# Optimization experiments

Measured on AMD Instinct MI355X. Metric: run time of the kernel, lower is better.

The kernel has to match this reference:

```python
import jax, jax.numpy as jnp
import numpy as np

N_E, E_DIM, N = 1024, 128, 262144


def setup_inputs() -> dict:
    key = jax.random.key(0)
    kx, kw = jax.random.split(key)
    x = jax.random.normal(kx, (N, E_DIM), dtype=jnp.float32)
    # nn.Embedding weight initialized uniform(-1/n_e, 1/n_e)
    W = jax.random.uniform(kw, (N_E, E_DIM), dtype=jnp.float32,
                           minval=-1.0 / N_E, maxval=1.0 / N_E)
    return {"x": x, "W": W}


def reference(x, W):
    # d[n, k] = ||x_n||^2 + ||W_k||^2 - 2 x_n . W_k   -> shape [N, n_e]
    d = (jnp.sum(x * x, axis=1, keepdims=True)
         + jnp.sum(W * W, axis=1)
         - 2.0 * jnp.matmul(x, W.T))
    min_indices = jnp.argmin(d, axis=1)          # [N] int
    z_q = jnp.take(W, min_indices, axis=0)       # [N, e_dim] gather
    return (z_q, min_indices)
```

## Files before the change

kernel.cpp:

```cpp
#include <hip/hip_runtime.h>

#define EDIM 128
#define NE   1024
#define TAU  5e-5f
#define CAPP 65536

typedef short v8s __attribute__((ext_vector_type(8)));
typedef float v4f __attribute__((ext_vector_type(4)));
typedef __attribute__((address_space(3))) void       lds_t;
typedef const __attribute__((address_space(1))) void gm_t;

__device__ inline unsigned bf16_rne(float f) {
    unsigned u = __float_as_uint(f);
    return (u + 0x7fffu + ((u >> 16) & 1u)) >> 16;
}
__device__ inline float bf16_tof(unsigned h) { return __uint_as_float(h << 16); }

__global__ void vq_prep(const float* __restrict__ W,
                        unsigned short* __restrict__ whiF,
                        unsigned short* __restrict__ wloF,
                        float* __restrict__ Wt,
                        float* __restrict__ swsq_ws)
{
#pragma clang fp contract(off)
    const int t = blockIdx.x * 256 + threadIdx.x;
    #pragma unroll
    for (int rep = 0; rep < 2; ++rep) {
        int i = t + rep * 65536;
        float v = W[i];
        int code = i >> 7, k = i & 127;
        int sub = code >> 4, m = code & 15;
        int ks = k >> 5, g = (k >> 3) & 3, e = k & 7;
        int o = sub * 2048 + ks * 512 + (g * 16 + m) * 8 + e;
        unsigned h = bf16_rne(v);
        whiF[o] = (unsigned short)h;
        wloF[o] = (unsigned short)bf16_rne(v - bf16_tof(h));
        int o2 = t + rep * 65536;
        Wt[o2] = W[(o2 & 1023) * EDIM + (o2 >> 10)];
    }
    if (t < NE) {
        const float4* wr = reinterpret_cast<const float4*>(W) + (size_t)t * 32;
        float4 A = wr[0], B = wr[1];
        float r0 = A.x*A.x, r1 = A.y*A.y, r2 = A.z*A.z, r3 = A.w*A.w;
        float r4 = B.x*B.x, r5 = B.y*B.y, r6 = B.z*B.z, r7 = B.w*B.w;
        #pragma unroll
        for (int i = 2; i < 32; i += 2) {
            float4 C = wr[i], D = wr[i + 1];
            r0 += C.x*C.x; r1 += C.y*C.y; r2 += C.z*C.z; r3 += C.w*C.w;
            r4 += D.x*D.x; r5 += D.y*D.y; r6 += D.z*D.z; r7 += D.w*D.w;
        }
        swsq_ws[t] = ((r0 + r1) + (r2 + r3)) + ((r4 + r5) + (r6 + r7));
    }
}

union SMem {
    struct { unsigned short ring[3][2][4096]; float snwk2h[NE]; } p1;
    struct { float4 scan[2048]; int sbest[128]; } p2;
};

__global__ __launch_bounds__(256, 3) void vq_mfma9(
    const float* __restrict__ x,
    const unsigned short* __restrict__ whiF, const unsigned short* __restrict__ wloF,
    const float* __restrict__ W, const float* __restrict__ swsq_ws,
    float* __restrict__ zq, float* __restrict__ idxout,
    int* __restrict__ cnt_pair, int* __restrict__ cnt_full,
    int* __restrict__ plist, int* __restrict__ flist)
{
    __shared__ SMem sm;

    const int tid = threadIdx.x;
    const int wid = tid >> 6;
    const int l   = tid & 63;
    const int m   = l & 15;
    const int g   = l >> 4;

    const long long row0 = (long long)blockIdx.x * 128;
    const float4* x4 = reinterpret_cast<const float4*>(x);
    const float4* W4 = reinterpret_cast<const float4*>(W);

#define STAGE_TILE(T, B) do {                                                          \
    __builtin_amdgcn_global_load_lds((gm_t*)(whiF + (size_t)(T) * 4096 + tid * 8),     \
        (lds_t*)&sm.p1.ring[B][0][tid * 8], 16, 0, 0);                                 \
    __builtin_amdgcn_global_load_lds((gm_t*)(whiF + (size_t)(T) * 4096 + 2048 + tid * 8), \
        (lds_t*)&sm.p1.ring[B][0][2048 + tid * 8], 16, 0, 0);                          \
    __builtin_amdgcn_global_load_lds((gm_t*)(wloF + (size_t)(T) * 4096 + tid * 8),     \
        (lds_t*)&sm.p1.ring[B][1][tid * 8], 16, 0, 0);                                 \
    __builtin_amdgcn_global_load_lds((gm_t*)(wloF + (size_t)(T) * 4096 + 2048 + tid * 8), \
        (lds_t*)&sm.p1.ring[B][1][2048 + tid * 8], 16, 0, 0);                          \
} while (0)

    STAGE_TILE(0, 0);
    STAGE_TILE(1, 1);

    {
        float4 v = reinterpret_cast<const float4*>(swsq_ws)[tid];
        v.x *= -0.5f; v.y *= -0.5f; v.z *= -0.5f; v.w *= -0.5f;
        reinterpret_cast<float4*>(sm.p1.snwk2h)[tid] = v;
    }

    const long long rA0 = row0 + wid * 32 + m;
    const long long rA1 = rA0 + 16;
    v8s a0h[4], a0l[4], a1h[4], a1l[4];
    #pragma unroll
    for (int ks = 0; ks < 4; ++ks) {
        float4 p0 = x4[rA0 * 32 + ks * 8 + g * 2];
        float4 p1 = x4[rA0 * 32 + ks * 8 + g * 2 + 1];
        float4 q0 = x4[rA1 * 32 + ks * 8 + g * 2];
        float4 q1 = x4[rA1 * 32 + ks * 8 + g * 2 + 1];
        float vp[8] = {p0.x,p0.y,p0.z,p0.w,p1.x,p1.y,p1.z,p1.w};
        float vq[8] = {q0.x,q0.y,q0.z,q0.w,q1.x,q1.y,q1.z,q1.w};
        #pragma unroll
        for (int e = 0; e < 8; ++e) {
            unsigned h0 = bf16_rne(vp[e]);
            a0h[ks][e] = (short)h0;
            a0l[ks][e] = (short)bf16_rne(vp[e] - bf16_tof(h0));
            unsigned h1 = bf16_rne(vq[e]);
            a1h[ks][e] = (short)h1;
            a1l[ks][e] = (short)bf16_rne(vq[e] - bf16_tof(h1));
        }
    }
    __syncthreads();

    float best[8], sec[8]; int bk[8];
    #pragma unroll
    for (int r = 0; r < 8; ++r) { best[r] = -3.4e38f; sec[r] = -3.4e38f; bk[r] = 0; }

    int bcur = 0;
    #pragma unroll 1
    for (int t = 0; t < 32; ++t) {
        if (t + 1 < 32) asm volatile("s_waitcnt vmcnt(4)" ::: "memory");
        else            asm volatile("s_waitcnt vmcnt(0)" ::: "memory");
        __builtin_amdgcn_s_barrier();

        if (t + 2 < 32) {
            int bnext = bcur + 2; if (bnext >= 3) bnext -= 3;
            STAGE_TILE(t + 2, bnext);
        }

        const unsigned short* bh_base = &sm.p1.ring[bcur][0][l * 8];
        const unsigned short* bl_base = &sm.p1.ring[bcur][1][l * 8];

        #pragma unroll
        for (int half = 0; half < 2; ++half) {
            const int k = t * 32 + half * 16 + m;
            const int hb = half * 2048;
            v8s bh0 = *(const v8s*)(bh_base + hb);
            v8s bh1 = *(const v8s*)(bh_base + hb + 512);
            v8s bh2 = *(const v8s*)(bh_base + hb + 1024);
            v8s bh3 = *(const v8s*)(bh_base + hb + 1536);
            v8s bl0 = *(const v8s*)(bl_base + hb);
            v8s bl1 = *(const v8s*)(bl_base + hb + 512);
            v8s bl2 = *(const v8s*)(bl_base + hb + 1024);
            v8s bl3 = *(const v8s*)(bl_base + hb + 1536);

            const float h = sm.p1.snwk2h[k];
            v4f acc0 = {h, h, h, h};
            v4f acc1 = {h, h, h, h};
            __builtin_amdgcn_s_setprio(1);
            acc0 = __builtin_amdgcn_mfma_f32_16x16x32_bf16(a0h[0], bh0, acc0, 0, 0, 0);
            acc0 = __builtin_amdgcn_mfma_f32_16x16x32_bf16(a0l[0], bh0, acc0, 0, 0, 0);
            acc0 = __builtin_amdgcn_mfma_f32_16x16x32_bf16(a0h[0], bl0, acc0, 0, 0, 0);
            acc1 = __builtin_amdgcn_mfma_f32_16x16x32_bf16(a1h[0], bh0, acc1, 0, 0, 0);
            acc1 = __builtin_amdgcn_mfma_f32_16x16x32_bf16(a1l[0], bh0, acc1, 0, 0, 0);
            acc1 = __builtin_amdgcn_mfma_f32_16x16x32_bf16(a1h[0], bl0, acc1, 0, 0, 0);
            acc0 = __builtin_amdgcn_mfma_f32_16x16x32_bf16(a0h[1], bh1, acc0, 0, 0, 0);
            acc0 = __builtin_amdgcn_mfma_f32_16x16x32_bf16(a0l[1], bh1, acc0, 0, 0, 0);
            acc0 = __builtin_amdgcn_mfma_f32_16x16x32_bf16(a0h[1], bl1, acc0, 0, 0, 0);
            acc1 = __builtin_amdgcn_mfma_f32_16x16x32_bf16(a1h[1], bh1, acc1, 0, 0, 0);
            acc1 = __builtin_amdgcn_mfma_f32_16x16x32_bf16(a1l[1], bh1, acc1, 0, 0, 0);
            acc1 = __builtin_amdgcn_mfma_f32_16x16x32_bf16(a1h[1], bl1, acc1, 0, 0, 0);
            acc0 = __builtin_amdgcn_mfma_f32_16x16x32_bf16(a0h[2], bh2, acc0, 0, 0, 0);
            acc0 = __builtin_amdgcn_mfma_f32_16x16x32_bf16(a0l[2], bh2, acc0, 0, 0, 0);
            acc0 = __builtin_amdgcn_mfma_f32_16x16x32_bf16(a0h[2], bl2, acc0, 0, 0, 0);
            acc1 = __builtin_amdgcn_mfma_f32_16x16x32_bf16(a1h[2], bh2, acc1, 0, 0, 0);
            acc1 = __builtin_amdgcn_mfma_f32_16x16x32_bf16(a1l[2], bh2, acc1, 0, 0, 0);
            acc1 = __builtin_amdgcn_mfma_f32_16x16x32_bf16(a1h[2], bl2, acc1, 0, 0, 0);
            acc0 = __builtin_amdgcn_mfma_f32_16x16x32_bf16(a0h[3], bh3, acc0, 0, 0, 0);
            acc0 = __builtin_amdgcn_mfma_f32_16x16x32_bf16(a0l[3], bh3, acc0, 0, 0, 0);
            acc0 = __builtin_amdgcn_mfma_f32_16x16x32_bf16(a0h[3], bl3, acc0, 0, 0, 0);
            acc1 = __builtin_amdgcn_mfma_f32_16x16x32_bf16(a1h[3], bh3, acc1, 0, 0, 0);
            acc1 = __builtin_amdgcn_mfma_f32_16x16x32_bf16(a1l[3], bh3, acc1, 0, 0, 0);
            acc1 = __builtin_amdgcn_mfma_f32_16x16x32_bf16(a1h[3], bl3, acc1, 0, 0, 0);
            __builtin_amdgcn_s_setprio(0);

            #pragma unroll
            for (int r = 0; r < 4; ++r) {
                float b0 = best[r];
                float a0r = acc0[r];
                sec[r]  = __builtin_amdgcn_fmed3f(a0r, b0, sec[r]);
                bk[r]   = (a0r > b0) ? k : bk[r];
                best[r] = fmaxf(b0, a0r);
                float b1 = best[4 + r];
                float a1r = acc1[r];
                sec[4+r]  = __builtin_amdgcn_fmed3f(a1r, b1, sec[4+r]);
                bk[4+r]   = (a1r > b1) ? k : bk[4+r];
                best[4+r] = fmaxf(b1, a1r);
            }
        }

        bcur = (bcur == 2) ? 0 : bcur + 1;
    }
    __syncthreads();

    #pragma unroll
    for (int r = 0; r < 8; ++r) {
        int rowL = wid * 32 + ((r >> 2) << 4) + (g << 2) + (r & 3);
        float4 e;
        e.x = -2.f * best[r]; e.y = -2.f * sec[r];
        e.z = __int_as_float(bk[r]); e.w = 0.f;
        sm.p2.scan[rowL * 16 + m] = e;
    }
    __syncthreads();

    if (tid < 128) {
        const int stag = tid & 7;
        float b1 = 3.4e38f; int k1 = 0x7fffffff;
        #pragma unroll 1
        for (int mm = 0; mm < 16; ++mm) {
            float4 e = sm.p2.scan[tid * 16 + (mm ^ stag)];
            int kk = __float_as_int(e.z);
            if (e.x < b1 || (e.x == b1 && kk < k1)) { b1 = e.x; k1 = kk; }
        }
        const float th = b1 + TAU;
        int nb = 0; bool asec = false;
        float b2 = 3.4e38f; int k2 = 0x7fffffff;
        #pragma unroll 1
        for (int mm = 0; mm < 16; ++mm) {
            float4 e = sm.p2.scan[tid * 16 + (mm ^ stag)];
            int kk = __float_as_int(e.z);
            nb  += (e.x <= th) ? 1 : 0;
            asec = asec || (e.y <= th);
            if (kk != k1 && (e.x < b2 || (e.x == b2 && kk < k2))) { b2 = e.x; k2 = kk; }
        }
        sm.p2.sbest[tid] = k1;
        idxout[row0 + tid] = (float)k1;
        const int row = (int)(row0 + tid);
        if (asec || nb > 2) {
            int s2 = atomicAdd(cnt_full, 1);
            flist[s2] = row;
        } else if (nb == 2) {
            int slot = atomicAdd(cnt_pair, 1);
            if (slot < CAPP) { plist[2 * slot] = row; plist[2 * slot + 1] = k2; }
            else { int s2 = atomicAdd(cnt_full, 1); flist[s2] = row; }
        }
    }
    __syncthreads();

    float4* zq4 = reinterpret_cast<float4*>(zq);
    for (int i = tid; i < 128 * 32; i += 256) {
        int r = i >> 5, c4 = i & 31;
        zq4[row0 * 32 + i] = W4[(size_t)sm.p2.sbest[r] * 32 + c4];
    }
#undef STAGE_TILE
}

__global__ __launch_bounds__(256, 4) void vq_fix(
    const float* __restrict__ x, const float* __restrict__ W,
    const float* __restrict__ Wt, const float* __restrict__ swsq_ws,
    float* __restrict__ zq, float* __restrict__ idxout,
    const int* __restrict__ cnt_pair, const int* __restrict__ plist,
    const int* __restrict__ cnt_full, const int* __restrict__ flist)
{
#pragma clang fp contract(off)
    const float4* W4 = reinterpret_cast<const float4*>(W);
    float4* zq4 = reinterpret_cast<float4*>(zq);

    {
        int n = *cnt_pair; if (n > CAPP) n = CAPP;
        const int gsz = gridDim.x * 256;
        for (int i = blockIdx.x * 256 + threadIdx.x; i < n; i += gsz) {
            const int row = plist[2 * i];
            const int k2  = plist[2 * i + 1];
            const int k1  = (int)idxout[row];
            const float4* xr4 = reinterpret_cast<const float4*>(x + (size_t)row * EDIM);
            float4 A = xr4[0], B = xr4[1];
            float r0 = A.x*A.x, r1 = A.y*A.y, r2 = A.z*A.z, r3 = A.w*A.w;
            float r4 = B.x*B.x, r5 = B.y*B.y, r6 = B.z*B.z, r7 = B.w*B.w;
            #pragma unroll
            for (int q = 2; q < 32; q += 2) {
                float4 C = xr4[q], D = xr4[q + 1];
                r0 += C.x*C.x; r1 += C.y*C.y; r2 += C.z*C.z; r3 += C.w*C.w;
                r4 += D.x*D.x; r5 += D.y*D.y; r6 += D.z*D.z; r7 += D.w*D.w;
            }
            float xxv = ((r0 + r1) + (r2 + r3)) + ((r4 + r5) + (r6 + r7));
            const float* xr = x + (size_t)row * EDIM;
            const float* w1 = W + (size_t)k1 * EDIM;
            const float* w2 = W + (size_t)k2 * EDIM;
            float dot1 = 0.f, dot2 = 0.f;
            #pragma unroll 4
            for (int j = 0; j < EDIM; ++j) {
                float a = xr[j];
                dot1 = fmaf(a, w1[j], dot1);
                dot2 = fmaf(a, w2[j], dot2);
            }
            float d1 = (xxv + swsq_ws[k1]) - (dot1 + dot1);
            float d2 = (xxv + swsq_ws[k2]) - (dot2 + dot2);
            int kw = (d2 < d1 || (d2 == d1 && k2 < k1)) ? k2 : k1;
            if (kw != k1) {
                idxout[row] = (float)kw;
                const float4* wr = W4 + (size_t)kw * 32;
                float4* zr = zq4 + (size_t)row * 32;
                #pragma unroll
                for (int q = 0; q < 32; ++q) zr[q] = wr[q];
            }
        }
    }

    {
        const int nf = *cnt_full;
        const int lane = threadIdx.x & 63;
        const int nw = gridDim.x * 4;
        const float4* Wt4 = reinterpret_cast<const float4*>(Wt);
        for (int i = blockIdx.x * 4 + (threadIdx.x >> 6); i < nf; i += nw) {
            const long long row = flist[i];
            const float4* xr4 = reinterpret_cast<const float4*>(x + row * EDIM);
            float xxv;
            {
                float4 A = xr4[0], B = xr4[1];
                float r0 = A.x*A.x, r1 = A.y*A.y, r2 = A.z*A.z, r3 = A.w*A.w;
                float r4 = B.x*B.x, r5 = B.y*B.y, r6 = B.z*B.z, r7 = B.w*B.w;
                #pragma unroll
                for (int q = 2; q < 32; q += 2) {
                    float4 C = xr4[q], D = xr4[q + 1];
                    r0 += C.x*C.x; r1 += C.y*C.y; r2 += C.z*C.z; r3 += C.w*C.w;
                    r4 += D.x*D.x; r5 += D.y*D.y; r6 += D.z*D.z; r7 += D.w*D.w;
                }
                xxv = ((r0 + r1) + (r2 + r3)) + ((r4 + r5) + (r6 + r7));
            }
            float acc[4][4];
            #pragma unroll
            for (int c = 0; c < 4; ++c)
                #pragma unroll
                for (int e = 0; e < 4; ++e) acc[c][e] = 0.f;
            const float* xr = x + row * EDIM;
            #pragma unroll 4
            for (int j = 0; j < EDIM; ++j) {
                float a = xr[j];
                #pragma unroll
                for (int c = 0; c < 4; ++c) {
                    float4 w = Wt4[(size_t)j * 256 + c * 64 + lane];
                    acc[c][0] = fmaf(a, w.x, acc[c][0]);
                    acc[c][1] = fmaf(a, w.y, acc[c][1]);
                    acc[c][2] = fmaf(a, w.z, acc[c][2]);
                    acc[c][3] = fmaf(a, w.w, acc[c][3]);
                }
            }
            float dbest = 3.4e38f; int bkk = 0;
            #pragma unroll
            for (int c = 0; c < 4; ++c)
                #pragma unroll
                for (int e = 0; e < 4; ++e) {
                    int k = c * 256 + lane * 4 + e;
                    float t1 = xxv + swsq_ws[k];
                    float d  = t1 - (acc[c][e] + acc[c][e]);
                    if (d < dbest) { dbest = d; bkk = k; }
                }
            #pragma unroll
            for (int mk = 1; mk < 64; mk <<= 1) {
                float od = __shfl_xor(dbest, mk);
                int   ok = __shfl_xor(bkk, mk);
                if (od < dbest || (od == dbest && ok < bkk)) { dbest = od; bkk = ok; }
            }
            if (lane == 0) idxout[row] = (float)bkk;
            if (lane < 32) zq4[row * 32 + lane] = W4[(size_t)bkk * 32 + lane];
        }
    }
}

__global__ __launch_bounds__(64, 2) void vq_v4(
    const float* __restrict__ x, const float* __restrict__ W,
    float* __restrict__ zq, float* __restrict__ idxout)
{
#pragma clang fp contract(off)
    __shared__ float swsq[NE];
    __shared__ int   sbest[64];
    const int tid = threadIdx.x;
    const long long row0 = (long long)blockIdx.x * 64;
    const long long row  = row0 + tid;
    const float4* x4 = reinterpret_cast<const float4*>(x);
    const float4* W4 = reinterpret_cast<const float4*>(W);
    float4 xr[32];
    #pragma unroll
    for (int i = 0; i < 32; ++i) xr[i] = x4[row * 32 + i];
    #pragma unroll
    for (int i = 0; i < 32; ++i)
        asm volatile("" : "+v"(xr[i].x), "+v"(xr[i].y), "+v"(xr[i].z), "+v"(xr[i].w));
    for (int k = tid; k < NE; k += 64) {
        const float4* wr = W4 + (size_t)k * 32;
        float4 A = wr[0], B = wr[1];
        float r0 = A.x*A.x, r1 = A.y*A.y, r2 = A.z*A.z, r3 = A.w*A.w;
        float r4 = B.x*B.x, r5 = B.y*B.y, r6 = B.z*B.z, r7 = B.w*B.w;
        #pragma unroll
        for (int i = 2; i < 32; i += 2) {
            float4 C = wr[i], D = wr[i + 1];
            r0 += C.x*C.x; r1 += C.y*C.y; r2 += C.z*C.z; r3 += C.w*C.w;
            r4 += D.x*D.x; r5 += D.y*D.y; r6 += D.z*D.z; r7 += D.w*D.w;
        }
        swsq[k] = ((r0 + r1) + (r2 + r3)) + ((r4 + r5) + (r6 + r7));
    }
    float xxv;
    {
        float r0 = xr[0].x*xr[0].x, r1 = xr[0].y*xr[0].y;
        float r2 = xr[0].z*xr[0].z, r3 = xr[0].w*xr[0].w;
        float r4 = xr[1].x*xr[1].x, r5 = xr[1].y*xr[1].y;
        float r6 = xr[1].z*xr[1].z, r7 = xr[1].w*xr[1].w;
        #pragma unroll
        for (int i = 2; i < 32; i += 2) {
            r0 += xr[i].x*xr[i].x;     r1 += xr[i].y*xr[i].y;
            r2 += xr[i].z*xr[i].z;     r3 += xr[i].w*xr[i].w;
            r4 += xr[i+1].x*xr[i+1].x; r5 += xr[i+1].y*xr[i+1].y;
            r6 += xr[i+1].z*xr[i+1].z; r7 += xr[i+1].w*xr[i+1].w;
        }
        xxv = ((r0 + r1) + (r2 + r3)) + ((r4 + r5) + (r6 + r7));
    }
    __syncthreads();
    float dbest = 3.4e38f; int bestk = 0;
    #pragma unroll 1
    for (int k0 = 0; k0 < NE; k0 += 8) {
        float acc[8];
        #pragma unroll
        for (int c = 0; c < 8; ++c) acc[c] = 0.f;
        #pragma unroll
        for (int j4 = 0; j4 < 32; ++j4) {
            const float4 a = xr[j4];
            #pragma unroll
            for (int c = 0; c < 8; ++c) {
                float4 w = W4[(size_t)(k0 + c) * 32 + j4];
                acc[c] = fmaf(a.x, w.x, acc[c]); acc[c] = fmaf(a.y, w.y, acc[c]);
                acc[c] = fmaf(a.z, w.z, acc[c]); acc[c] = fmaf(a.w, w.w, acc[c]);
            }
        }
        #pragma unroll
        for (int c = 0; c < 8; ++c) {
            float t1 = xxv + swsq[k0 + c];
            float d  = t1 - (acc[c] + acc[c]);
            if (d < dbest) { dbest = d; bestk = k0 + c; }
        }
    }
    sbest[tid] = bestk;
    idxout[row] = (float)bestk;
    __syncthreads();
    float4* zq4 = reinterpret_cast<float4*>(zq);
    for (int i = tid; i < 64 * 32; i += 64) {
        int r = i >> 5, c4 = i & 31;
        zq4[row0 * 32 + i] = W4[(size_t)sbest[r] * 32 + c4];
    }
}

extern "C" void kernel_launch(void* const* d_in, const int* in_sizes, int n_in,
                              void* d_out, int out_size, void* d_ws, size_t ws_size,
                              hipStream_t stream) {
    (void)n_in; (void)out_size;
    const float* x = (const float*)d_in[0];
    const float* W = (const float*)d_in[1];
    const int Nrows = in_sizes[0] / EDIM;

    float* zqp    = (float*)d_out;
    float* idxout = zqp + (size_t)Nrows * EDIM;

    const size_t need = 16 + 2 * (size_t)NE * EDIM * 2 + NE * 4
                      + (size_t)NE * EDIM * 4 + (size_t)CAPP * 2 * 4
                      + (size_t)Nrows * 4;
    if (ws_size < need) {
        vq_v4<<<dim3(Nrows / 64), dim3(64), 0, stream>>>(x, W, zqp, idxout);
        return;
    }

    char* p = (char*)d_ws;
    int*            cnt_pair = (int*)p;
    int*            cnt_full = (int*)(p + 4);
    unsigned short* whiF  = (unsigned short*)(p + 16);
    unsigned short* wloF  = whiF + NE * EDIM;
    float*          swsqw = (float*)(wloF + NE * EDIM);
    float*          Wt    = swsqw + NE;
    int*            plist = (int*)(Wt + NE * EDIM);
    int*            flist = plist + CAPP * 2;

    hipMemsetAsync(d_ws, 0, 16, stream);
    vq_prep<<<dim3(256), dim3(256), 0, stream>>>(W, whiF, wloF, Wt, swsqw);
    vq_mfma9<<<dim3(Nrows / 128), dim3(256), 0, stream>>>(x, whiF, wloF, W, swsqw,
                                                          zqp, idxout,
                                                          cnt_pair, cnt_full,
                                                          plist, flist);
    vq_fix<<<dim3(1024), dim3(256), 0, stream>>>(x, W, Wt, swsqw, zqp, idxout,
                                                 cnt_pair, plist, cnt_full, flist);
}
```

Baseline: 330.9 us.

## Halve codebook tile size to raise occupancy and coalesce prep layout writes

The main kernel now stages 16 codes per pipeline step instead of 32, halving the LDS ring and shrinking the argmin scratch (float4 to float2 plus a separate int array), so launch bounds can request 4 blocks per CU instead of 3. The loop runs 64 iterations with one MFMA group each, which doubles the barrier and wait overhead per code. Separately, the prep kernel builds the bf16 hi/lo swizzled layout through shared memory with vector stores instead of scattered 2-byte global writes. Fewer registers may be available per thread under the higher occupancy target.

```diff
diff --git a/kernel.cpp b/kernel.cpp
--- a/kernel.cpp
+++ b/kernel.cpp
@@ -23,21 +23,38 @@
                         float* __restrict__ swsq_ws)
 {
 #pragma clang fp contract(off)
-    const int t = blockIdx.x * 256 + threadIdx.x;
+    __shared__ unsigned short lh[2048], ll[2048];
+    const int tid = threadIdx.x;
+    const int t = blockIdx.x * 256 + tid;
+
+    if (blockIdx.x < 64) {
+        const int sub = blockIdx.x;
+        const int dst = ((tid & 15) >> 2) * 512 + (tid & 3) * 128 + (tid >> 4) * 8;
+        float4 p0 = reinterpret_cast<const float4*>(W)[sub * 512 + tid * 2];
+        float4 p1 = reinterpret_cast<const float4*>(W)[sub * 512 + tid * 2 + 1];
+        float v[8] = {p0.x,p0.y,p0.z,p0.w,p1.x,p1.y,p1.z,p1.w};
+        v8s hh, llw;
+        #pragma unroll
+        for (int j = 0; j < 8; ++j) {
+            unsigned h = bf16_rne(v[j]);
+            hh[j]  = (short)h;
+            llw[j] = (short)bf16_rne(v[j] - bf16_tof(h));
+        }
+        *reinterpret_cast<v8s*>(&lh[dst]) = hh;
+        *reinterpret_cast<v8s*>(&ll[dst]) = llw;
+        __syncthreads();
+        *reinterpret_cast<v8s*>(&whiF[sub * 2048 + tid * 8]) =
+            *reinterpret_cast<const v8s*>(&lh[tid * 8]);
+        *reinterpret_cast<v8s*>(&wloF[sub * 2048 + tid * 8]) =
+            *reinterpret_cast<const v8s*>(&ll[tid * 8]);
+    }
+
     #pragma unroll
     for (int rep = 0; rep < 2; ++rep) {
-        int i = t + rep * 65536;
-        float v = W[i];
-        int code = i >> 7, k = i & 127;
-        int sub = code >> 4, m = code & 15;
-        int ks = k >> 5, g = (k >> 3) & 3, e = k & 7;
-        int o = sub * 2048 + ks * 512 + (g * 16 + m) * 8 + e;
-        unsigned h = bf16_rne(v);
-        whiF[o] = (unsigned short)h;
-        wloF[o] = (unsigned short)bf16_rne(v - bf16_tof(h));
         int o2 = t + rep * 65536;
         Wt[o2] = W[(o2 & 1023) * EDIM + (o2 >> 10)];
     }
+
     if (t < NE) {
         const float4* wr = reinterpret_cast<const float4*>(W) + (size_t)t * 32;
         float4 A = wr[0], B = wr[1];
@@ -54,11 +71,11 @@
 }
 
 union SMem {
-    struct { unsigned short ring[3][2][4096]; float snwk2h[NE]; } p1;
-    struct { float4 scan[2048]; int sbest[128]; } p2;
+    struct { unsigned short ring[3][2][2048]; float snwk2h[NE]; } p1;
+    struct { float2 sbs[2048]; int sbk[2048]; int sbest[128]; } p2;
 };
 
-__global__ __launch_bounds__(256, 3) void vq_mfma9(
+__global__ __launch_bounds__(256, 4) void vq_mfma12(
     const float* __restrict__ x,
     const unsigned short* __restrict__ whiF, const unsigned short* __restrict__ wloF,
     const float* __restrict__ W, const float* __restrict__ swsq_ws,
@@ -79,14 +96,10 @@
     const float4* W4 = reinterpret_cast<const float4*>(W);
 
 #define STAGE_TILE(T, B) do {                                                          \
-    __builtin_amdgcn_global_load_lds((gm_t*)(whiF + (size_t)(T) * 4096 + tid * 8),     \
+    __builtin_amdgcn_global_load_lds((gm_t*)(whiF + (size_t)(T) * 2048 + tid * 8),     \
         (lds_t*)&sm.p1.ring[B][0][tid * 8], 16, 0, 0);                                 \
-    __builtin_amdgcn_global_load_lds((gm_t*)(whiF + (size_t)(T) * 4096 + 2048 + tid * 8), \
-        (lds_t*)&sm.p1.ring[B][0][2048 + tid * 8], 16, 0, 0);                          \
-    __builtin_amdgcn_global_load_lds((gm_t*)(wloF + (size_t)(T) * 4096 + tid * 8),     \
+    __builtin_amdgcn_global_load_lds((gm_t*)(wloF + (size_t)(T) * 2048 + tid * 8),     \
         (lds_t*)&sm.p1.ring[B][1][tid * 8], 16, 0, 0);                                 \
-    __builtin_amdgcn_global_load_lds((gm_t*)(wloF + (size_t)(T) * 4096 + 2048 + tid * 8), \
-        (lds_t*)&sm.p1.ring[B][1][2048 + tid * 8], 16, 0, 0);                          \
 } while (0)
 
     STAGE_TILE(0, 0);
@@ -127,75 +140,70 @@
 
     int bcur = 0;
     #pragma unroll 1
-    for (int t = 0; t < 32; ++t) {
-        if (t + 1 < 32) asm volatile("s_waitcnt vmcnt(4)" ::: "memory");
+    for (int t = 0; t < 64; ++t) {
+        if (t + 1 < 64) asm volatile("s_waitcnt vmcnt(2)" ::: "memory");
         else            asm volatile("s_waitcnt vmcnt(0)" ::: "memory");
         __builtin_amdgcn_s_barrier();
 
-        if (t + 2 < 32) {
+        if (t + 2 < 64) {
             int bnext = bcur + 2; if (bnext >= 3) bnext -= 3;
             STAGE_TILE(t + 2, bnext);
         }
 
         const unsigned short* bh_base = &sm.p1.ring[bcur][0][l * 8];
         const unsigned short* bl_base = &sm.p1.ring[bcur][1][l * 8];
-
-        #pragma unroll
-        for (int half = 0; half < 2; ++half) {
-            const int k = t * 32 + half * 16 + m;
-            const int hb = half * 2048;
-            v8s bh0 = *(const v8s*)(bh_base + hb);
-            v8s bh1 = *(const v8s*)(bh_base + hb + 512);
-            v8s bh2 = *(const v8s*)(bh_base + hb + 1024);
-            v8s bh3 = *(const v8s*)(bh_base + hb + 1536);
-            v8s bl0 = *(const v8s*)(bl_base + hb);
-            v8s bl1 = *(const v8s*)(bl_base + hb + 512);
-            v8s bl2 = *(const v8s*)(bl_base + hb + 1024);
-            v8s bl3 = *(const v8s*)(bl_base + hb + 1536);
-
-            const float h = sm.p1.snwk2h[k];
-            v4f acc0 = {h, h, h, h};
-            v4f acc1 = {h, h, h, h};
-            __builtin_amdgcn_s_setprio(1);
-            acc0 = __builtin_amdgcn_mfma_f32_16x16x32_bf16(a0h[0], bh0, acc0, 0, 0, 0);
-            acc0 = __builtin_amdgcn_mfma_f32_16x16x32_bf16(a0l[0], bh0, acc0, 0, 0, 0);
-            acc0 = __builtin_amdgcn_mfma_f32_16x16x32_bf16(a0h[0], bl0, acc0, 0, 0, 0);
-            acc1 = __builtin_amdgcn_mfma_f32_16x16x32_bf16(a1h[0], bh0, acc1, 0, 0, 0);
-            acc1 = __builtin_amdgcn_mfma_f32_16x16x32_bf16(a1l[0], bh0, acc1, 0, 0, 0);
-            acc1 = __builtin_amdgcn_mfma_f32_16x16x32_bf16(a1h[0], bl0, acc1, 0, 0, 0);
-            acc0 = __builtin_amdgcn_mfma_f32_16x16x32_bf16(a0h[1], bh1, acc0, 0, 0, 0);
-            acc0 = __builtin_amdgcn_mfma_f32_16x16x32_bf16(a0l[1], bh1, acc0, 0, 0, 0);
-            acc0 = __builtin_amdgcn_mfma_f32_16x16x32_bf16(a0h[1], bl1, acc0, 0, 0, 0);
-            acc1 = __builtin_amdgcn_mfma_f32_16x16x32_bf16(a1h[1], bh1, acc1, 0, 0, 0);
-            acc1 = __builtin_amdgcn_mfma_f32_16x16x32_bf16(a1l[1], bh1, acc1, 0, 0, 0);
-            acc1 = __builtin_amdgcn_mfma_f32_16x16x32_bf16(a1h[1], bl1, acc1, 0, 0, 0);
-            acc0 = __builtin_amdgcn_mfma_f32_16x16x32_bf16(a0h[2], bh2, acc0, 0, 0, 0);
-            acc0 = __builtin_amdgcn_mfma_f32_16x16x32_bf16(a0l[2], bh2, acc0, 0, 0, 0);
-            acc0 = __builtin_amdgcn_mfma_f32_16x16x32_bf16(a0h[2], bl2, acc0, 0, 0, 0);
-            acc1 = __builtin_amdgcn_mfma_f32_16x16x32_bf16(a1h[2], bh2, acc1, 0, 0, 0);
-            acc1 = __builtin_amdgcn_mfma_f32_16x16x32_bf16(a1l[2], bh2, acc1, 0, 0, 0);
-            acc1 = __builtin_amdgcn_mfma_f32_16x16x32_bf16(a1h[2], bl2, acc1, 0, 0, 0);
-            acc0 = __builtin_amdgcn_mfma_f32_16x16x32_bf16(a0h[3], bh3, acc0, 0, 0, 0);
-            acc0 = __builtin_amdgcn_mfma_f32_16x16x32_bf16(a0l[3], bh3, acc0, 0, 0, 0);
-            acc0 = __builtin_amdgcn_mfma_f32_16x16x32_bf16(a0h[3], bl3, acc0, 0, 0, 0);
-            acc1 = __builtin_amdgcn_mfma_f32_16x16x32_bf16(a1h[3], bh3, acc1, 0, 0, 0);
-            acc1 = __builtin_amdgcn_mfma_f32_16x16x32_bf16(a1l[3], bh3, acc1, 0, 0, 0);
-            acc1 = __builtin_amdgcn_mfma_f32_16x16x32_bf16(a1h[3], bl3, acc1, 0, 0, 0);
-            __builtin_amdgcn_s_setprio(0);
-
-            #pragma unroll
-            for (int r = 0; r < 4; ++r) {
-                float b0 = best[r];
-                float a0r = acc0[r];
-                sec[r]  = __builtin_amdgcn_fmed3f(a0r, b0, sec[r]);
-                bk[r]   = (a0r > b0) ? k : bk[r];
-                best[r] = fmaxf(b0, a0r);
-                float b1 = best[4 + r];
-                float a1r = acc1[r];
-                sec[4+r]  = __builtin_amdgcn_fmed3f(a1r, b1, sec[4+r]);
-                bk[4+r]   = (a1r > b1) ? k : bk[4+r];
-                best[4+r] = fmaxf(b1, a1r);
-            }
+        v8s bh0 = *(const v8s*)(bh_base);
+        v8s bh1 = *(const v8s*)(bh_base + 512);
+        v8s bh2 = *(const v8s*)(bh_base + 1024);
+        v8s bh3 = *(const v8s*)(bh_base + 1536);
+        v8s bl0 = *(const v8s*)(bl_base);
+        v8s bl1 = *(const v8s*)(bl_base + 512);
+        v8s bl2 = *(const v8s*)(bl_base + 1024);
+        v8s bl3 = *(const v8s*)(bl_base + 1536);
+
+        const int k = t * 16 + m;
+        const float h = sm.p1.snwk2h[k];
+        v4f acc0 = {h, h, h, h};
+        v4f acc1 = {h, h, h, h};
+        __builtin_amdgcn_s_setprio(1);
+        acc0 = __builtin_amdgcn_mfma_f32_16x16x32_bf16(a0h[0], bh0, acc0, 0, 0, 0);
+        acc0 = __builtin_amdgcn_mfma_f32_16x16x32_bf16(a0l[0], bh0, acc0, 0, 0, 0);
+        acc0 = __builtin_amdgcn_mfma_f32_16x16x32_bf16(a0h[0], bl0, acc0, 0, 0, 0);
+        acc1 = __builtin_amdgcn_mfma_f32_16x16x32_bf16(a1h[0], bh0, acc1, 0, 0, 0);
+        acc1 = __builtin_amdgcn_mfma_f32_16x16x32_bf16(a1l[0], bh0, acc1, 0, 0, 0);
+        acc1 = __builtin_amdgcn_mfma_f32_16x16x32_bf16(a1h[0], bl0, acc1, 0, 0, 0);
+        acc0 = __builtin_amdgcn_mfma_f32_16x16x32_bf16(a0h[1], bh1, acc0, 0, 0, 0);
+        acc0 = __builtin_amdgcn_mfma_f32_16x16x32_bf16(a0l[1], bh1, acc0, 0, 0, 0);
+        acc0 = __builtin_amdgcn_mfma_f32_16x16x32_bf16(a0h[1], bl1, acc0, 0, 0, 0);
+        acc1 = __builtin_amdgcn_mfma_f32_16x16x32_bf16(a1h[1], bh1, acc1, 0, 0, 0);
+        acc1 = __builtin_amdgcn_mfma_f32_16x16x32_bf16(a1l[1], bh1, acc1, 0, 0, 0);
+        acc1 = __builtin_amdgcn_mfma_f32_16x16x32_bf16(a1h[1], bl1, acc1, 0, 0, 0);
+        acc0 = __builtin_amdgcn_mfma_f32_16x16x32_bf16(a0h[2], bh2, acc0, 0, 0, 0);
+        acc0 = __builtin_amdgcn_mfma_f32_16x16x32_bf16(a0l[2], bh2, acc0, 0, 0, 0);
+        acc0 = __builtin_amdgcn_mfma_f32_16x16x32_bf16(a0h[2], bl2, acc0, 0, 0, 0);
+        acc1 = __builtin_amdgcn_mfma_f32_16x16x32_bf16(a1h[2], bh2, acc1, 0, 0, 0);
+        acc1 = __builtin_amdgcn_mfma_f32_16x16x32_bf16(a1l[2], bh2, acc1, 0, 0, 0);
+        acc1 = __builtin_amdgcn_mfma_f32_16x16x32_bf16(a1h[2], bl2, acc1, 0, 0, 0);
+        acc0 = __builtin_amdgcn_mfma_f32_16x16x32_bf16(a0h[3], bh3, acc0, 0, 0, 0);
+        acc0 = __builtin_amdgcn_mfma_f32_16x16x32_bf16(a0l[3], bh3, acc0, 0, 0, 0);
+        acc0 = __builtin_amdgcn_mfma_f32_16x16x32_bf16(a0h[3], bl3, acc0, 0, 0, 0);
+        acc1 = __builtin_amdgcn_mfma_f32_16x16x32_bf16(a1h[3], bh3, acc1, 0, 0, 0);
+        acc1 = __builtin_amdgcn_mfma_f32_16x16x32_bf16(a1l[3], bh3, acc1, 0, 0, 0);
+        acc1 = __builtin_amdgcn_mfma_f32_16x16x32_bf16(a1h[3], bl3, acc1, 0, 0, 0);
+        __builtin_amdgcn_s_setprio(0);
+
+        #pragma unroll
+        for (int r = 0; r < 4; ++r) {
+            float b0 = best[r];
+            float a0r = acc0[r];
+            sec[r]  = __builtin_amdgcn_fmed3f(a0r, b0, sec[r]);
+            bk[r]   = (a0r > b0) ? k : bk[r];
+            best[r] = fmaxf(b0, a0r);
+            float b1 = best[4 + r];
+            float a1r = acc1[r];
+            sec[4+r]  = __builtin_amdgcn_fmed3f(a1r, b1, sec[4+r]);
+            bk[4+r]   = (a1r > b1) ? k : bk[4+r];
+            best[4+r] = fmaxf(b1, a1r);
         }
 
         bcur = (bcur == 2) ? 0 : bcur + 1;
@@ -205,10 +213,9 @@
     #pragma unroll
     for (int r = 0; r < 8; ++r) {
         int rowL = wid * 32 + ((r >> 2) << 4) + (g << 2) + (r & 3);
-        float4 e;
-        e.x = -2.f * best[r]; e.y = -2.f * sec[r];
-        e.z = __int_as_float(bk[r]); e.w = 0.f;
-        sm.p2.scan[rowL * 16 + m] = e;
+        float2 e; e.x = -2.f * best[r]; e.y = -2.f * sec[r];
+        sm.p2.sbs[rowL * 16 + m] = e;
+        sm.p2.sbk[rowL * 16 + m] = bk[r];
     }
     __syncthreads();
 
@@ -217,8 +224,9 @@
         float b1 = 3.4e38f; int k1 = 0x7fffffff;
         #pragma unroll 1
         for (int mm = 0; mm < 16; ++mm) {
-            float4 e = sm.p2.scan[tid * 16 + (mm ^ stag)];
-            int kk = __float_as_int(e.z);
+            int idx = tid * 16 + (mm ^ stag);
+            float2 e = sm.p2.sbs[idx];
+            int kk = sm.p2.sbk[idx];
             if (e.x < b1 || (e.x == b1 && kk < k1)) { b1 = e.x; k1 = kk; }
         }
         const float th = b1 + TAU;
@@ -226,8 +234,9 @@
         float b2 = 3.4e38f; int k2 = 0x7fffffff;
         #pragma unroll 1
         for (int mm = 0; mm < 16; ++mm) {
-            float4 e = sm.p2.scan[tid * 16 + (mm ^ stag)];
-            int kk = __float_as_int(e.z);
+            int idx = tid * 16 + (mm ^ stag);
+            float2 e = sm.p2.sbs[idx];
+            int kk = sm.p2.sbk[idx];
             nb  += (e.x <= th) ? 1 : 0;
             asec = asec || (e.y <= th);
             if (kk != k1 && (e.x < b2 || (e.x == b2 && kk < k2))) { b2 = e.x; k2 = kk; }
@@ -478,10 +487,10 @@
 
     hipMemsetAsync(d_ws, 0, 16, stream);
     vq_prep<<<dim3(256), dim3(256), 0, stream>>>(W, whiF, wloF, Wt, swsqw);
-    vq_mfma9<<<dim3(Nrows / 128), dim3(256), 0, stream>>>(x, whiF, wloF, W, swsqw,
-                                                          zqp, idxout,
-                                                          cnt_pair, cnt_full,
-                                                          plist, flist);
+    vq_mfma12<<<dim3(Nrows / 128), dim3(256), 0, stream>>>(x, whiF, wloF, W, swsqw,
+                                                           zqp, idxout,
+                                                           cnt_pair, cnt_full,
+                                                           plist, flist);
     vq_fix<<<dim3(1024), dim3(256), 0, stream>>>(x, W, Wt, swsqw, zqp, idxout,
                                                  cnt_pair, plist, cnt_full, flist);
 }
```

Result: slower. 497.1 us (+50.2%).
